# Optimization experiments

Measured on AMD Instinct MI355X. Metric: run time of the kernel, lower is better.

## Reference

```python
import jax, jax.numpy as jnp
import numpy as np

D, H, W = 160, 192, 160


def _grid_sample_3d(vol, grid):
    """torch F.grid_sample (3D, bilinear/trilinear, padding='zeros', align_corners=False).
    vol: [B,C,D,H,W]; grid: [B,Do,Ho,Wo,3], last dim ordered (x,y,z) in [-1,1]."""
    B, C, Dv, Hv, Wv = vol.shape
    x, y, z = grid[..., 0], grid[..., 1], grid[..., 2]
    # align_corners=False unnormalization
    ix = ((x + 1.0) * Wv - 1.0) * 0.5
    iy = ((y + 1.0) * Hv - 1.0) * 0.5
    iz = ((z + 1.0) * Dv - 1.0) * 0.5
    fx, fy, fz = jnp.floor(ix), jnp.floor(iy), jnp.floor(iz)
    wx, wy, wz = ix - fx, iy - fy, iz - fz
    ix0, iy0, iz0 = fx.astype(jnp.int32), fy.astype(jnp.int32), fz.astype(jnp.int32)
    vol_flat = vol.reshape(B, C, Dv * Hv * Wv)
    out_sp = x.shape[1:]  # (Do, Ho, Wo)

    def gather(zi, yi, xi):
        inb = ((zi >= 0) & (zi < Dv) & (yi >= 0) & (yi < Hv) & (xi >= 0) & (xi < Wv))
        lin = ((jnp.clip(zi, 0, Dv - 1) * Hv + jnp.clip(yi, 0, Hv - 1)) * Wv
               + jnp.clip(xi, 0, Wv - 1)).reshape(B, -1)
        vals = jax.vmap(lambda v, i: v[:, i])(vol_flat, lin)  # [B,C,N]
        return vals.reshape((B, C) + out_sp) * inb[:, None].astype(vol.dtype)

    out = jnp.zeros((B, C) + tuple(out_sp), vol.dtype)
    # fixed 8-corner trilinear accumulation
    for dz, wz_ in ((0, 1.0 - wz), (1, wz)):
        for dy, wy_ in ((0, 1.0 - wy), (1, wy)):
            for dx, wx_ in ((0, 1.0 - wx), (1, wx)):
                w = (wz_ * wy_ * wx_)[:, None]  # [B,1,Do,Ho,Wo]
                out = out + w * gather(iz0 + dz, iy0 + dy, ix0 + dx)
    return out


def _voxel_grid():
    gd, gh, gw = jnp.meshgrid(jnp.arange(D, dtype=jnp.float32),
                              jnp.arange(H, dtype=jnp.float32),
                              jnp.arange(W, dtype=jnp.float32), indexing='ij')
    return jnp.stack([gd, gh, gw])[None]  # [1,3,D,H,W], channels (d,h,w)


def _to_xyz(t):
    # [B,3,D,H,W] channels (d,h,w) -> [B,D,H,W,3] channels (x,y,z)
    return jnp.moveaxis(t, 1, -1)[..., ::-1]


def setup_inputs() -> dict:
    key = jax.random.key(0)
    k1, k2, k3 = jax.random.split(key, 3)
    src = jax.random.normal(k1, (1, 1, D, H, W), dtype=jnp.float32)
    flow1 = jax.random.normal(k2, (1, 3, D, H, W), dtype=jnp.float32)
    flow2 = jax.random.normal(k3, (1, 3, D, H, W), dtype=jnp.float32)
    range_flow = jnp.float32(0.4)
    return {"src": src, "flow1": flow1, "flow2": flow2, "range_flow": range_flow}


def reference(src, flow1, flow2, range_flow):
    grid = _voxel_grid()  # voxel-coordinate identity grid
    # NOTE: grid2 is intentionally NOT normalized to [-1,1] (faithful to source quirk)
    grid2 = _to_xyz(grid + flow2 * range_flow)
    flow1_warped = _grid_sample_3d(flow1, grid2)
    out_flow = flow1_warped + flow2
    denom = jnp.array([D - 1, H - 1, W - 1], jnp.float32).reshape(1, 3, 1, 1, 1)
    new_locs_total = 2.0 * ((grid + out_flow * range_flow) / denom - 0.5)
    deform_2_img = _grid_sample_3d(src, _to_xyz(new_locs_total))
    return deform_2_img, out_flow
```

## Files before the change

kernel.cpp:

```cpp
#include <hip/hip_runtime.h>

constexpr int Dv = 160, Hv = 192, Wv = 160;
constexpr int NN = Dv * Hv * Wv;

constexpr int TW = 32, TH = 8, TD = 8;

__device__ __forceinline__ void tri3_rare(const float* __restrict__ v,
                                          float gx, float gy, float gz,
                                          float& o0, float& o1, float& o2) {
  o0 = 0.0f; o1 = 0.0f; o2 = 0.0f;
  float ix = ((gx + 1.0f) * (float)Wv - 1.0f) * 0.5f;
  float iy = ((gy + 1.0f) * (float)Hv - 1.0f) * 0.5f;
  float iz = ((gz + 1.0f) * (float)Dv - 1.0f) * 0.5f;
  float fx = floorf(ix), fy = floorf(iy), fz = floorf(iz);
  int x0 = (int)fx, y0 = (int)fy, z0 = (int)fz;
  if (x0 < -1 || x0 >= Wv || y0 < -1 || y0 >= Hv || z0 < -1 || z0 >= Dv)
    return;
  float wx = ix - fx, wy = iy - fy, wz = iz - fz;
#pragma unroll
  for (int c = 0; c < 8; ++c) {
    const int dz = (c >> 2) & 1, dy = (c >> 1) & 1, dx = c & 1;
    int zi = z0 + dz, yi = y0 + dy, xi = x0 + dx;
    if ((unsigned)zi < (unsigned)Dv && (unsigned)yi < (unsigned)Hv &&
        (unsigned)xi < (unsigned)Wv) {
      float wgt = (dz ? wz : 1.0f - wz) * (dy ? wy : 1.0f - wy) *
                  (dx ? wx : 1.0f - wx);
      int lin = (zi * Hv + yi) * Wv + xi;
      o0 += wgt * v[lin];
      o1 += wgt * v[NN + lin];
      o2 += wgt * v[2 * NN + lin];
    }
  }
}

__global__ __launch_bounds__(256)
void st_gather_kernel(const float* __restrict__ src,
                      const float* __restrict__ flow1,
                      const float* __restrict__ flow2,
                      const float* __restrict__ rfp,
                      float* __restrict__ out) {
  const int tid = threadIdx.x;
  const int bx0 = blockIdx.x * TW;
  const int by0 = blockIdx.y * TH;
  const int bz0 = blockIdx.z * TD;
  const float rf = rfp[0];

  const int lx = tid & 7;
  const int ly = (tid >> 3) & 7;
  const int lz = tid >> 6;
  const int w0 = bx0 + lx * 4;
  const int h = by0 + ly;

  float4 f2d4[2], f2h4[2], f2w4[2];
#pragma unroll
  for (int s = 0; s < 2; ++s) {
    int d = bz0 + 2 * lz + s;
    int idx = (d * Hv + h) * Wv + w0;
    f2d4[s] = *(const float4*)(flow2 + idx);
    f2h4[s] = *(const float4*)(flow2 + NN + idx);
    f2w4[s] = *(const float4*)(flow2 + 2 * NN + idx);
  }

  const float hf = (float)h;
  constexpr float KX = (float)Wv / (float)(Wv - 1);
  constexpr float KY = (float)Hv / (float)(Hv - 1);
  constexpr float KZ = (float)Dv / (float)(Dv - 1);

#pragma unroll
  for (int s = 0; s < 2; ++s) {
    const int d = bz0 + 2 * lz + s;
    const float df = (float)d;
    const int idx = (d * Hv + h) * Wv + w0;

    float4 def, ofd4, ofh4, ofw4;
#pragma unroll
    for (int j = 0; j < 4; ++j) {
      const float wf = (float)(w0 + j);
      const float f2dv = (&f2d4[s].x)[j];
      const float f2hv = (&f2h4[s].x)[j];
      const float f2wv = (&f2w4[s].x)[j];

      float a0, a1, a2;
      tri3_rare(flow1, wf + rf * f2wv, hf + rf * f2hv, df + rf * f2dv,
                a0, a1, a2);

      float of_d = a0 + f2dv;
      float of_h = a1 + f2hv;
      float of_w = a2 + f2wv;
      (&ofd4.x)[j] = of_d;
      (&ofh4.x)[j] = of_h;
      (&ofw4.x)[j] = of_w;

      float ix = (wf + rf * of_w) * KX - 0.5f;
      float iy = (hf + rf * of_h) * KY - 0.5f;
      float iz = (df + rf * of_d) * KZ - 0.5f;

      float fx = floorf(ix), fy = floorf(iy), fz = floorf(iz);
      float wx = ix - fx, wy = iy - fy, wz = iz - fz;
      int x0 = (int)fx, y0 = (int)fy, z0 = (int)fz;

      float wx0 = ((unsigned)x0 < (unsigned)Wv) ? (1.0f - wx) : 0.0f;
      float wx1 = ((unsigned)(x0 + 1) < (unsigned)Wv) ? wx : 0.0f;
      float wy0 = ((unsigned)y0 < (unsigned)Hv) ? (1.0f - wy) : 0.0f;
      float wy1 = ((unsigned)(y0 + 1) < (unsigned)Hv) ? wy : 0.0f;
      float wz0 = ((unsigned)z0 < (unsigned)Dv) ? (1.0f - wz) : 0.0f;
      float wz1 = ((unsigned)(z0 + 1) < (unsigned)Dv) ? wz : 0.0f;

      int xa0 = min(max(x0, 0), Wv - 1), xa1 = min(max(x0 + 1, 0), Wv - 1);
      int ya0 = min(max(y0, 0), Hv - 1), ya1 = min(max(y0 + 1, 0), Hv - 1);
      int za0 = min(max(z0, 0), Dv - 1), za1 = min(max(z0 + 1, 0), Dv - 1);

      int r00 = (za0 * Hv + ya0) * Wv;
      int r01 = (za0 * Hv + ya1) * Wv;
      int r10 = (za1 * Hv + ya0) * Wv;
      int r11 = (za1 * Hv + ya1) * Wv;
      float v000 = src[r00 + xa0], v001 = src[r00 + xa1];
      float v010 = src[r01 + xa0], v011 = src[r01 + xa1];
      float v100 = src[r10 + xa0], v101 = src[r10 + xa1];
      float v110 = src[r11 + xa0], v111 = src[r11 + xa1];

      float c00 = v000 * wx0 + v001 * wx1;
      float c01 = v010 * wx0 + v011 * wx1;
      float c10 = v100 * wx0 + v101 * wx1;
      float c11 = v110 * wx0 + v111 * wx1;
      float c0 = c00 * wy0 + c01 * wy1;
      float c1 = c10 * wy0 + c11 * wy1;
      (&def.x)[j] = c0 * wz0 + c1 * wz1;
    }

    *(float4*)(out + idx) = def;
    *(float4*)(out + NN + idx) = ofd4;
    *(float4*)(out + 2 * NN + idx) = ofh4;
    *(float4*)(out + 3 * NN + idx) = ofw4;
  }
}

extern "C" void kernel_launch(void* const* d_in, const int* in_sizes, int n_in,
                              void* d_out, int out_size, void* d_ws, size_t ws_size,
                              hipStream_t stream) {
  const float* src   = (const float*)d_in[0];
  const float* flow1 = (const float*)d_in[1];
  const float* flow2 = (const float*)d_in[2];
  const float* rfp   = (const float*)d_in[3];
  float* out = (float*)d_out;

  dim3 grid(Wv / TW, Hv / TH, Dv / TD);
  hipLaunchKernelGGL(st_gather_kernel, grid, dim3(256), 0, stream,
                     src, flow1, flow2, rfp, out);
}
```

Before: 198.0 us.

## Stage src halo tiles in LDS with async pipelined loads along depth

Each block now walks four depth steps of 4 slices and streams padded src slabs into a 4-slot LDS ring using global_load_lds, prefetching ahead while it computes and also double-buffering the flow2 loads. The trilinear gather reads its 8 corners from LDS when the sample lands inside the staged halo and falls back to global loads otherwise. A 1D grid with a swizzled block order replaces the 3D grid. The aim is to cut scattered global gather traffic and hide load latency, at the cost of hand-tuned vmcnt waits, barriers, extra LDS use, and correctness that depends on exact wait counts.

After: 181.7 us. -8.2%, faster.

```diff
diff --git a/kernel.cpp b/kernel.cpp
--- a/kernel.cpp
+++ b/kernel.cpp
@@ -3,7 +3,39 @@
 constexpr int Dv = 160, Hv = 192, Wv = 160;
 constexpr int NN = Dv * Hv * Wv;
 
-constexpr int TW = 32, TH = 8, TD = 8;
+constexpr int TW = 32, TH = 8, TDS = 4;
+constexpr int NSTEP = 4;
+constexpr int SX = 40, SY = 12;
+constexpr int PLF = SX * SY;
+constexpr int GRF = PLF * 4;
+constexpr int GRSEG = GRF / 4;
+constexpr int LDSF = 4 * GRF;
+
+#define WAITV(n) asm volatile("s_waitcnt vmcnt(" #n ")" ::: "memory")
+
+__device__ __forceinline__ void stage_group(const float* __restrict__ src,
+                                            float* lds, int k, int bxo, int byo) {
+  const int tid = threadIdx.x;
+  float* base = lds + (k & 3) * GRF;
+  const int zb = k * 4;
+#pragma unroll
+  for (int i = 0; i < 2; ++i) {
+    const int t = tid + i * 256;
+    if (t < GRSEG) {
+      int p = t / 120;
+      int q = t - p * 120;
+      int ty = q / 10;
+      int tx4 = (q - ty * 10) * 4;
+      int gz = min(max(zb + p, 0), Dv - 1);
+      int gy = min(max(byo + ty, 0), Hv - 1);
+      int gx = min(max(bxo + tx4, 0), Wv - 4);
+      int g = (gz * Hv + gy) * Wv + gx;
+      __builtin_amdgcn_global_load_lds(
+          (const __attribute__((address_space(1))) void*)(src + g),
+          (__attribute__((address_space(3))) void*)(base + t * 4), 16, 0, 0);
+    }
+  }
+}
 
 __device__ __forceinline__ void tri3_rare(const float* __restrict__ v,
                                           float gx, float gy, float gz,
@@ -34,32 +66,42 @@
 }
 
 __global__ __launch_bounds__(256)
-void st_gather_kernel(const float* __restrict__ src,
-                      const float* __restrict__ flow1,
-                      const float* __restrict__ flow2,
-                      const float* __restrict__ rfp,
-                      float* __restrict__ out) {
+void st_pipe_kernel(const float* __restrict__ src,
+                    const float* __restrict__ flow1,
+                    const float* __restrict__ flow2,
+                    const float* __restrict__ rfp,
+                    float* __restrict__ out) {
+  __shared__ float tile[LDSF];
+
   const int tid = threadIdx.x;
-  const int bx0 = blockIdx.x * TW;
-  const int by0 = blockIdx.y * TH;
-  const int bz0 = blockIdx.z * TD;
   const float rf = rfp[0];
 
-  const int lx = tid & 7;
-  const int ly = (tid >> 3) & 7;
-  const int lz = tid >> 6;
+  const int bid = (int)blockIdx.x;
+  const int swz = (bid & 7) * 150 + (bid >> 3);
+  const int bx = swz % 5;
+  const int t1 = swz / 5;
+  const int by = t1 % 24;
+  const int bz = t1 / 24;
+
+  const int bx0 = bx * TW, by0 = by * TH;
+  const int zbase = bz * (TDS * NSTEP);
+  const int k0 = bz * NSTEP;
+  const int bxo = bx0 - 4, byo = by0 - 2;
+
+  stage_group(src, tile, k0 - 1, bxo, byo);
+  stage_group(src, tile, k0,     bxo, byo);
+  stage_group(src, tile, k0 + 1, bxo, byo);
+
+  const int lx = tid & 7, ly = (tid >> 3) & 7, lz = tid >> 6;
   const int w0 = bx0 + lx * 4;
   const int h = by0 + ly;
-
-  float4 f2d4[2], f2h4[2], f2w4[2];
-#pragma unroll
-  for (int s = 0; s < 2; ++s) {
-    int d = bz0 + 2 * lz + s;
-    int idx = (d * Hv + h) * Wv + w0;
-    f2d4[s] = *(const float4*)(flow2 + idx);
-    f2h4[s] = *(const float4*)(flow2 + NN + idx);
-    f2w4[s] = *(const float4*)(flow2 + 2 * NN + idx);
-  }
+  const int idx0 = ((zbase + lz) * Hv + h) * Wv + w0;
+  constexpr int ZSTRIDE = TDS * Hv * Wv;
+
+  float4 f2d[2], f2h[2], f2w[2];
+  f2d[0] = *(const float4*)(flow2 + idx0);
+  f2h[0] = *(const float4*)(flow2 + NN + idx0);
+  f2w[0] = *(const float4*)(flow2 + 2 * NN + idx0);
 
   const float hf = (float)h;
   constexpr float KX = (float)Wv / (float)(Wv - 1);
@@ -67,18 +109,36 @@
   constexpr float KZ = (float)Dv / (float)(Dv - 1);
 
 #pragma unroll
-  for (int s = 0; s < 2; ++s) {
-    const int d = bz0 + 2 * lz + s;
+  for (int s = 0; s < NSTEP; ++s) {
+    const int cur = s & 1, nxt = cur ^ 1;
+
+    if (s + 2 <= NSTEP)
+      stage_group(src, tile, k0 + 2 + s, bxo, byo);
+    if (s + 1 < NSTEP) {
+      const int idxn = idx0 + (s + 1) * ZSTRIDE;
+      f2d[nxt] = *(const float4*)(flow2 + idxn);
+      f2h[nxt] = *(const float4*)(flow2 + NN + idxn);
+      f2w[nxt] = *(const float4*)(flow2 + 2 * NN + idxn);
+    }
+
+    if (s == 0)            WAITV(5);
+    else if (s == NSTEP-1) WAITV(4);
+    else                   WAITV(9);
+    __builtin_amdgcn_sched_barrier(0);
+    __builtin_amdgcn_s_barrier();
+
+    const int a = zbase + TDS * s;
+    const int d = a + lz;
     const float df = (float)d;
-    const int idx = (d * Hv + h) * Wv + w0;
+    const int idx = idx0 + s * ZSTRIDE;
 
     float4 def, ofd4, ofh4, ofw4;
 #pragma unroll
     for (int j = 0; j < 4; ++j) {
       const float wf = (float)(w0 + j);
-      const float f2dv = (&f2d4[s].x)[j];
-      const float f2hv = (&f2h4[s].x)[j];
-      const float f2wv = (&f2w4[s].x)[j];
+      const float f2dv = (&f2d[cur].x)[j];
+      const float f2hv = (&f2h[cur].x)[j];
+      const float f2wv = (&f2w[cur].x)[j];
 
       float a0, a1, a2;
       tri3_rare(flow1, wf + rf * f2wv, hf + rf * f2hv, df + rf * f2dv,
@@ -106,18 +166,34 @@
       float wz0 = ((unsigned)z0 < (unsigned)Dv) ? (1.0f - wz) : 0.0f;
       float wz1 = ((unsigned)(z0 + 1) < (unsigned)Dv) ? wz : 0.0f;
 
-      int xa0 = min(max(x0, 0), Wv - 1), xa1 = min(max(x0 + 1, 0), Wv - 1);
-      int ya0 = min(max(y0, 0), Hv - 1), ya1 = min(max(y0 + 1, 0), Hv - 1);
-      int za0 = min(max(z0, 0), Dv - 1), za1 = min(max(z0 + 1, 0), Dv - 1);
-
-      int r00 = (za0 * Hv + ya0) * Wv;
-      int r01 = (za0 * Hv + ya1) * Wv;
-      int r10 = (za1 * Hv + ya0) * Wv;
-      int r11 = (za1 * Hv + ya1) * Wv;
-      float v000 = src[r00 + xa0], v001 = src[r00 + xa1];
-      float v010 = src[r01 + xa0], v011 = src[r01 + xa1];
-      float v100 = src[r10 + xa0], v101 = src[r10 + xa1];
-      float v110 = src[r11 + xa0], v111 = src[r11 + xa1];
+      int txi = x0 - bxo, tyi = y0 - byo, tzi = z0 - (a - 2);
+      bool fast = ((unsigned)txi <= (unsigned)(SX - 2)) &
+                  ((unsigned)tyi <= (unsigned)(SY - 2)) &
+                  ((unsigned)tzi <= 7u);
+
+      float v000, v001, v010, v011, v100, v101, v110, v111;
+      if (fast) {
+        int yx = tyi * SX + txi;
+        int z1 = z0 + 1;
+        int b0 = ((z0 >> 2) & 3) * GRF + (z0 & 3) * PLF + yx;
+        int b1 = ((z1 >> 2) & 3) * GRF + (z1 & 3) * PLF + yx;
+        v000 = tile[b0];      v001 = tile[b0 + 1];
+        v010 = tile[b0 + SX]; v011 = tile[b0 + SX + 1];
+        v100 = tile[b1];      v101 = tile[b1 + 1];
+        v110 = tile[b1 + SX]; v111 = tile[b1 + SX + 1];
+      } else {
+        int xa0 = min(max(x0, 0), Wv - 1), xa1 = min(max(x0 + 1, 0), Wv - 1);
+        int ya0 = min(max(y0, 0), Hv - 1), ya1 = min(max(y0 + 1, 0), Hv - 1);
+        int za0 = min(max(z0, 0), Dv - 1), za1 = min(max(z0 + 1, 0), Dv - 1);
+        int r00 = (za0 * Hv + ya0) * Wv;
+        int r01 = (za0 * Hv + ya1) * Wv;
+        int r10 = (za1 * Hv + ya0) * Wv;
+        int r11 = (za1 * Hv + ya1) * Wv;
+        v000 = src[r00 + xa0]; v001 = src[r00 + xa1];
+        v010 = src[r01 + xa0]; v011 = src[r01 + xa1];
+        v100 = src[r10 + xa0]; v101 = src[r10 + xa1];
+        v110 = src[r11 + xa0]; v111 = src[r11 + xa1];
+      }
 
       float c00 = v000 * wx0 + v001 * wx1;
       float c01 = v010 * wx0 + v011 * wx1;
@@ -132,6 +208,9 @@
     *(float4*)(out + NN + idx) = ofd4;
     *(float4*)(out + 2 * NN + idx) = ofh4;
     *(float4*)(out + 3 * NN + idx) = ofw4;
+
+    __builtin_amdgcn_s_barrier();
+    __builtin_amdgcn_sched_barrier(0);
   }
 }
 
@@ -144,7 +223,6 @@
   const float* rfp   = (const float*)d_in[3];
   float* out = (float*)d_out;
 
-  dim3 grid(Wv / TW, Hv / TH, Dv / TD);
-  hipLaunchKernelGGL(st_gather_kernel, grid, dim3(256), 0, stream,
+  hipLaunchKernelGGL(st_pipe_kernel, dim3(1200), dim3(256), 0, stream,
                      src, flow1, flow2, rfp, out);
 }
```
